# Kernel optimization log

Measured on AMD Instinct MI355X. Metric: run time of the kernel, lower is better.

The kernel has to match this reference:

```python
import jax, jax.numpy as jnp
import numpy as np

V, CTX, D, L, H = 50257, 2048, 768, 12, 12
HD = D // H
EPS = 1e-5


def _ln(x, w, b):
    mu = jnp.mean(x, axis=-1, keepdims=True)
    var = jnp.mean(jnp.square(x - mu), axis=-1, keepdims=True)
    return (x - mu) * jax.lax.rsqrt(var + EPS) * w + b


def setup_inputs() -> dict:
    key = jax.random.key(0)
    ks = jax.random.split(key, 8)
    s = 0.02  # init std, matches _init_weights
    return {
        "idx": jax.random.randint(ks[0], (2, 2048), 0, V),
        "wte": jax.random.normal(ks[1], (V, D), jnp.float32) * s,
        "wpe": jax.random.normal(ks[2], (CTX, D), jnp.float32) * s,
        "ln1_w": jnp.ones((L, D), jnp.float32),
        "ln1_b": jnp.zeros((L, D), jnp.float32),
        "qkv_w": jax.random.normal(ks[3], (L, 3 * D, D), jnp.float32) * s,
        "out_w": jax.random.normal(ks[4], (L, D, D), jnp.float32) * s,
        "ln2_w": jnp.ones((L, D), jnp.float32),
        "ln2_b": jnp.zeros((L, D), jnp.float32),
        "fc1_w": jax.random.normal(ks[5], (L, 4 * D, D), jnp.float32) * s,
        "fc2_w": jax.random.normal(ks[6], (L, D, 4 * D), jnp.float32) * s,
        "lnf_w": jnp.ones((D,), jnp.float32),
        "lnf_b": jnp.zeros((D,), jnp.float32),
    }


def reference(idx, wte, wpe, ln1_w, ln1_b, qkv_w, out_w, ln2_w, ln2_b,
              fc1_w, fc2_w, lnf_w, lnf_b):
    B, S = idx.shape
    x = wte[idx] + wpe[:S][None]  # [B,S,D]
    causal = jnp.tril(jnp.ones((S, S), bool))  # [S,S]
    scale = 1.0 / np.sqrt(HD)

    def block(x, p):
        l1w, l1b, qkvw, ow, l2w, l2b, f1w, f2w = p
        h = _ln(x, l1w, l1b)
        qkv = h @ qkvw.T  # [B,S,3D]
        q, k, v = jnp.split(qkv, 3, axis=-1)
        q = q.reshape(B, S, H, HD)
        k = k.reshape(B, S, H, HD)
        v = v.reshape(B, S, H, HD)
        scores = jnp.einsum("bqhd,bkhd->bhqk", q, k) * scale
        scores = jnp.where(causal, scores, -jnp.inf)
        attn = jax.nn.softmax(scores, axis=-1)
        ctx = jnp.einsum("bhqk,bkhd->bqhd", attn, v).reshape(B, S, D)
        x = x + ctx @ ow.T
        h2 = _ln(x, l2w, l2b)
        mlp = jax.nn.gelu(h2 @ f1w.T, approximate=False) @ f2w.T
        return x + mlp, None

    x, _ = jax.lax.scan(block, x, (ln1_w, ln1_b, qkv_w, out_w, ln2_w, ln2_b, fc1_w, fc2_w))
    x = _ln(x, lnf_w, lnf_b)
    logits = x @ wte.T  # tied lm_head
    return logits
```

## Files before the change

### kernel.cpp

```cpp
#include <hip/hip_runtime.h>
#include <hip/hip_bf16.h>
#include <math.h>

typedef __attribute__((ext_vector_type(4))) float f32x4;
typedef __attribute__((ext_vector_type(8))) short bf16x8;
typedef __attribute__((ext_vector_type(4))) float float4v;
typedef unsigned short u16;
typedef unsigned int u32;

#define DIM 768
#define SEQ 2048
#define NTOK 4096
#define NH 12
#define NL 12
#define VOCAB 50257

__device__ __forceinline__ u16 f2bf(float f) {
  union { float f; u32 u; } c; c.f = f;
  u32 u = c.u;
  u32 r = u + 0x7fffu + ((u >> 16) & 1u);
  return (u16)(r >> 16);
}

__device__ __forceinline__ float fexp2(float x) {
#if __has_builtin(__builtin_amdgcn_exp2f)
  return __builtin_amdgcn_exp2f(x);
#else
  return exp2f(x);
#endif
}

__device__ __forceinline__ f32x4 mfma_bf16(bf16x8 a, bf16x8 b, f32x4 c) {
  return __builtin_amdgcn_mfma_f32_16x16x32_bf16(a, b, c, 0, 0, 0);
}

__device__ __forceinline__ void gload_lds16(const u16* g, u16* l) {
  __builtin_amdgcn_global_load_lds((const __attribute__((address_space(1))) u32*)g,
                                   (__attribute__((address_space(3))) u32*)l, 16, 0, 0);
}

__global__ void embed_k(const int* __restrict__ idx, const float* __restrict__ wte,
                        const float* __restrict__ wpe, float* __restrict__ x) {
  int t = blockIdx.x * 256 + threadIdx.x;
  int n = t / 192, c = t % 192;
  int tok = idx[n];
  float4v a = ((const float4v*)wte)[(size_t)tok * 192 + c];
  float4v p = ((const float4v*)wpe)[(size_t)(n & (SEQ - 1)) * 192 + c];
  ((float4v*)x)[t] = a + p;
}

__global__ __launch_bounds__(256) void ln_k(const float* __restrict__ x,
                                            const float* __restrict__ w,
                                            const float* __restrict__ b,
                                            u16* __restrict__ out) {
  int lane = threadIdx.x & 63;
  int row = blockIdx.x * 4 + (threadIdx.x >> 6);
  const float4v* xr = (const float4v*)(x + (size_t)row * DIM);
  float4v v[3];
#pragma unroll
  for (int i = 0; i < 3; ++i) v[i] = xr[i * 64 + lane];
  float s = 0.f;
#pragma unroll
  for (int i = 0; i < 3; ++i)
#pragma unroll
    for (int j = 0; j < 4; ++j) s += v[i][j];
#pragma unroll
  for (int o = 1; o < 64; o <<= 1) s += __shfl_xor(s, o);
  float mu = s * (1.f / 768.f);
  float vs = 0.f;
#pragma unroll
  for (int i = 0; i < 3; ++i)
#pragma unroll
    for (int j = 0; j < 4; ++j) { float d = v[i][j] - mu; vs += d * d; }
#pragma unroll
  for (int o = 1; o < 64; o <<= 1) vs += __shfl_xor(vs, o);
  float rs = rsqrtf(vs * (1.f / 768.f) + 1e-5f);
  u16* orow = out + (size_t)row * DIM;
#pragma unroll
  for (int i = 0; i < 3; ++i) {
    float4v wv = ((const float4v*)w)[i * 64 + lane];
    float4v bv = ((const float4v*)b)[i * 64 + lane];
    float y0 = (v[i][0] - mu) * rs * wv[0] + bv[0];
    float y1 = (v[i][1] - mu) * rs * wv[1] + bv[1];
    float y2 = (v[i][2] - mu) * rs * wv[2] + bv[2];
    float y3 = (v[i][3] - mu) * rs * wv[3] + bv[3];
    uint2 pk;
    pk.x = (u32)f2bf(y0) | ((u32)f2bf(y1) << 16);
    pk.y = (u32)f2bf(y2) | ((u32)f2bf(y3) << 16);
    ((uint2*)orow)[i * 64 + lane] = pk;
  }
}

__global__ void cvt_k(const float* __restrict__ src, u16* __restrict__ dst, int n4) {
  int stride = gridDim.x * blockDim.x;
  for (int i = blockIdx.x * blockDim.x + threadIdx.x; i < n4; i += stride) {
    float4v v = ((const float4v*)src)[i];
    uint2 pk;
    pk.x = (u32)f2bf(v[0]) | ((u32)f2bf(v[1]) << 16);
    pk.y = (u32)f2bf(v[2]) | ((u32)f2bf(v[3]) << 16);
    ((uint2*)dst)[i] = pk;
  }
}

template <int EPI>
__global__ __launch_bounds__(256) void gemm128p(const u16* __restrict__ A,
                                                const u16* __restrict__ W, int Mdim,
                                                int Kdim, u16* __restrict__ outb,
                                                float* __restrict__ resid) {
  __shared__ u16 lA[2][128 * 64];
  __shared__ u16 lW[2][128 * 64];
  const int m0 = blockIdx.y * 128;
  const int n0 = blockIdx.x * 128;
  const int tid = threadIdx.x;
  const int lane = tid & 63, wv = tid >> 6;
  const int wr = wv >> 1, wc = wv & 1;
  const int lr = lane & 15, hi = lane >> 4;

  f32x4 acc[4][4];
#pragma unroll
  for (int i = 0; i < 4; ++i)
#pragma unroll
    for (int j = 0; j < 4; ++j) acc[i][j] = (f32x4){0.f, 0.f, 0.f, 0.f};

  const int s_row = tid >> 3;
  const int s_col = (tid & 7) * 8;
  const int g_col = s_col ^ ((s_row & 7) << 3);
  int wrow[4];
#pragma unroll
  for (int it = 0; it < 4; ++it) {
    int r = m0 + s_row + it * 32;
    wrow[it] = (r < Mdim) ? r : (Mdim - 1);
  }

  const int nt = Kdim >> 6;

  auto stage = [&](int kt, int buf) {
    const int k0 = kt * 64;
#pragma unroll
    for (int it = 0; it < 4; ++it) {
      gload_lds16(A + (size_t)(n0 + s_row + it * 32) * Kdim + k0 + g_col,
                  &lA[buf][(s_row + it * 32) * 64 + s_col]);
      gload_lds16(W + (size_t)wrow[it] * Kdim + k0 + g_col,
                  &lW[buf][(s_row + it * 32) * 64 + s_col]);
    }
  };

  const int swz = (lr & 7) << 3;

  stage(0, 0);
  stage(1, 1);
  asm volatile("s_waitcnt vmcnt(8)" ::: "memory");
  __builtin_amdgcn_s_barrier();

  for (int t = 0; t < nt; ++t) {
    const int cur = t & 1;
    const u16* la = lA[cur];
    const u16* lw = lW[cur];
#pragma unroll
    for (int kk = 0; kk < 2; ++kk) {
      const int csw = (kk * 32 + hi * 8) ^ swz;
      bf16x8 af[4], wf[4];
#pragma unroll
      for (int i = 0; i < 4; ++i)
        af[i] = *(const bf16x8*)(&la[(wr * 64 + i * 16 + lr) * 64 + csw]);
#pragma unroll
      for (int j = 0; j < 4; ++j)
        wf[j] = *(const bf16x8*)(&lw[(wc * 64 + j * 16 + lr) * 64 + csw]);
      __builtin_amdgcn_s_setprio(1);
#pragma unroll
      for (int i = 0; i < 4; ++i)
#pragma unroll
        for (int j = 0; j < 4; ++j) acc[i][j] = mfma_bf16(af[i], wf[j], acc[i][j]);
      __builtin_amdgcn_s_setprio(0);
    }
    __builtin_amdgcn_s_barrier();
    if (t + 2 < nt) {
      stage(t + 2, cur);
      asm volatile("s_waitcnt vmcnt(8)" ::: "memory");
    } else if (t + 1 < nt) {
      asm volatile("s_waitcnt vmcnt(0)" ::: "memory");
    }
    __builtin_amdgcn_s_barrier();
  }

#pragma unroll
  for (int i = 0; i < 4; ++i) {
#pragma unroll
    for (int j = 0; j < 4; ++j) {
      int nb = n0 + wr * 64 + i * 16 + hi * 4;
      int m = m0 + wc * 64 + j * 16 + lr;
#pragma unroll
      for (int r = 0; r < 4; ++r) {
        float val = acc[i][j][r];
        size_t o = (size_t)(nb + r) * Mdim + m;
        if (EPI == 0) {
          if (m < Mdim) outb[o] = f2bf(val);
        } else if (EPI == 1) {
          float g = 0.5f * val * (1.f + erff(val * 0.70710678118f));
          outb[o] = f2bf(g);
        } else if (EPI == 2) {
          resid[o] += val;
        } else {
          if (m < Mdim) resid[o] = val;
        }
      }
    }
  }
}

template <int EPI>
__global__ __launch_bounds__(512) void gemm256(const u16* __restrict__ A,
                                               const u16* __restrict__ W, int Mdim,
                                               int Kdim, u16* __restrict__ outb,
                                               float* __restrict__ resid) {
  __shared__ u16 lA[2][256 * 64];
  __shared__ u16 lB[2][256 * 64];
  const int n0 = blockIdx.x * 256;
  const int m0 = blockIdx.y * 256;
  const int tid = threadIdx.x;
  const int lane = tid & 63, wid = tid >> 6;
  const int wr = wid >> 2, wc = wid & 3;
  const int lr = lane & 15, hi = lane >> 4;

  const int s_row = tid >> 3;
  const int s_col = (tid & 7) * 8;
  const int g_col = s_col ^ ((s_row & 7) << 3);
  int wrow[4];
#pragma unroll
  for (int it = 0; it < 4; ++it) {
    int r = m0 + s_row + it * 64;
    wrow[it] = (r < Mdim) ? r : (Mdim - 1);
  }

  f32x4 acc[8][4];
#pragma unroll
  for (int i = 0; i < 8; ++i)
#pragma unroll
    for (int j = 0; j < 4; ++j) acc[i][j] = (f32x4){0.f, 0.f, 0.f, 0.f};

  const int nt = Kdim >> 6;

  auto stage = [&](int kt, int buf) {
    const int k0 = kt * 64;
#pragma unroll
    for (int it = 0; it < 4; ++it)
      gload_lds16(A + (size_t)(n0 + s_row + it * 64) * Kdim + k0 + g_col,
                  &lA[buf][(s_row + it * 64) * 64 + s_col]);
#pragma unroll
    for (int it = 0; it < 4; ++it)
      gload_lds16(W + (size_t)wrow[it] * Kdim + k0 + g_col,
                  &lB[buf][(s_row + it * 64) * 64 + s_col]);
  };

  const int swz = (lr & 7) << 3;

  stage(0, 0);
  stage(1, 1);
  asm volatile("s_waitcnt vmcnt(8)" ::: "memory");
  __builtin_amdgcn_s_barrier();

  for (int t = 0; t < nt; ++t) {
    const int cur = t & 1;
    const u16* la = lA[cur];
    const u16* lb = lB[cur];
#pragma unroll
    for (int kk = 0; kk < 2; ++kk) {
      const int csw = (kk * 32 + hi * 8) ^ swz;
      bf16x8 af[8], wf[4];
#pragma unroll
      for (int i = 0; i < 8; ++i)
        af[i] = *(const bf16x8*)(&la[(wr * 128 + i * 16 + lr) * 64 + csw]);
#pragma unroll
      for (int j = 0; j < 4; ++j)
        wf[j] = *(const bf16x8*)(&lb[(wc * 64 + j * 16 + lr) * 64 + csw]);
      __builtin_amdgcn_s_setprio(1);
#pragma unroll
      for (int i = 0; i < 8; ++i)
#pragma unroll
        for (int j = 0; j < 4; ++j) acc[i][j] = mfma_bf16(af[i], wf[j], acc[i][j]);
      __builtin_amdgcn_s_setprio(0);
    }
    __builtin_amdgcn_s_barrier();
    if (t + 2 < nt) {
      stage(t + 2, cur);
      asm volatile("s_waitcnt vmcnt(8)" ::: "memory");
    } else if (t + 1 < nt) {
      asm volatile("s_waitcnt vmcnt(0)" ::: "memory");
    }
    __builtin_amdgcn_s_barrier();
  }

#pragma unroll
  for (int i = 0; i < 8; ++i) {
#pragma unroll
    for (int j = 0; j < 4; ++j) {
      int nb = n0 + wr * 128 + i * 16 + hi * 4;
      int m = m0 + wc * 64 + j * 16 + lr;
#pragma unroll
      for (int r = 0; r < 4; ++r) {
        float val = acc[i][j][r];
        size_t o = (size_t)(nb + r) * Mdim + m;
        if (EPI == 0) {
          if (m < Mdim) outb[o] = f2bf(val);
        } else if (EPI == 1) {
          float g = 0.5f * val * (1.f + erff(val * 0.70710678118f));
          outb[o] = f2bf(g);
        } else {
          if (m < Mdim) resid[o] = val;
        }
      }
    }
  }
}

__global__ __launch_bounds__(256) void vtrans_k(const u16* __restrict__ qkv,
                                                u16* __restrict__ vT) {
  __shared__ u16 t[64][65];
  int bh = blockIdx.y;
  int b = bh / NH, h = bh % NH;
  int s0 = blockIdx.x * 64;
  int tid = threadIdx.x;
  int col = tid & 63, row0 = tid >> 6;
#pragma unroll
  for (int it = 0; it < 16; ++it) {
    int srow = row0 + it * 4;
    t[srow][col] = qkv[(size_t)(b * SEQ + s0 + srow) * 2304 + 1536 + h * 64 + col];
  }
  __syncthreads();
#pragma unroll
  for (int it = 0; it < 16; ++it) {
    int drow = row0 + it * 4;
    vT[((size_t)bh * 64 + drow) * SEQ + s0 + col] = t[col][drow];
  }
}

__global__ __launch_bounds__(512) void flash_k(const u16* __restrict__ qkv,
                                               const u16* __restrict__ vT,
                                               u16* __restrict__ ctx) {
  const int tid = threadIdx.x;
  const int lane = tid & 63, wq = tid >> 6;
  const int lr = lane & 15, hi = lane >> 4;
  const int pi = blockIdx.x;
  const int bh = blockIdx.y;
  const int b = bh / NH, h = bh % NH;
  const size_t rowb = (size_t)b * SEQ;
  const float SCL = 0.125f * 1.44269504f;

  __shared__ u16 lK[64 * 80];
  __shared__ u16 lV[64 * 80];
  __shared__ u16 Pb[8][16 * 40];
  u16* P = Pb[wq];

  const int s_row = tid >> 3;
  const int s_col = (tid & 7) * 8;
  const u16* kSrc = qkv + rowb * 2304 + 768 + h * 64;
  const u16* vSrc = vT + ((size_t)bh * 64 + s_row) * SEQ;

#pragma unroll
  for (int pass = 0; pass < 2; ++pass) {
    const int qb = (pass == 0 ? (15 - pi) : pi) * 128;
    const int qa = qb + wq * 16;

    const u16* Qp = qkv + (rowb + qa + lr) * 2304 + h * 64 + hi * 8;
    bf16x8 qf0 = *(const bf16x8*)(Qp);
    bf16x8 qf1 = *(const bf16x8*)(Qp + 32);

    f32x4 o[4];
    float mreg[4], lreg[4];
#pragma unroll
    for (int ct = 0; ct < 4; ++ct) o[ct] = (f32x4){0.f, 0.f, 0.f, 0.f};
#pragma unroll
    for (int r = 0; r < 4; ++r) { mreg[r] = -1e30f; lreg[r] = 0.f; }

    const int kTop = qb + 127;
    bf16x8 kreg = *(const bf16x8*)(kSrc + (size_t)s_row * 2304 + s_col);
    bf16x8 vreg = *(const bf16x8*)(vSrc + s_col);

    for (int k0 = 0; k0 <= kTop; k0 += 64) {
      __syncthreads();
      *(bf16x8*)(&lK[s_row * 80 + s_col]) = kreg;
      *(bf16x8*)(&lV[s_row * 80 + s_col]) = vreg;
      __syncthreads();
      if (k0 + 64 <= kTop) {
        kreg = *(const bf16x8*)(kSrc + (size_t)(k0 + 64 + s_row) * 2304 + s_col);
        vreg = *(const bf16x8*)(vSrc + k0 + 64 + s_col);
      }
      if (k0 <= qa + 15) {
#pragma unroll
        for (int ks = 0; ks < 2; ++ks) {
          const int kg = k0 + ks * 32;
          f32x4 s0 = (f32x4){0.f, 0.f, 0.f, 0.f}, s1 = (f32x4){0.f, 0.f, 0.f, 0.f};
          {
            bf16x8 ka = *(const bf16x8*)(&lK[(ks * 32 + lr) * 80 + hi * 8]);
            bf16x8 kc = *(const bf16x8*)(&lK[(ks * 32 + lr) * 80 + hi * 8 + 32]);
            s0 = mfma_bf16(qf0, ka, s0);
            s0 = mfma_bf16(qf1, kc, s0);
            bf16x8 kd = *(const bf16x8*)(&lK[(ks * 32 + 16 + lr) * 80 + hi * 8]);
            bf16x8 ke = *(const bf16x8*)(&lK[(ks * 32 + 16 + lr) * 80 + hi * 8 + 32]);
            s1 = mfma_bf16(qf0, kd, s1);
            s1 = mfma_bf16(qf1, ke, s1);
          }
          float cor[4];
#pragma unroll
          for (int r = 0; r < 4; ++r) {
            int qrow = qa + hi * 4 + r;
            float v0 = s0[r] * SCL;
            if (kg + lr > qrow) v0 = -1e30f;
            float v1 = s1[r] * SCL;
            if (kg + 16 + lr > qrow) v1 = -1e30f;
            s0[r] = v0; s1[r] = v1;
            float m = fmaxf(v0, v1);
            m = fmaxf(m, __shfl_xor(m, 1));
            m = fmaxf(m, __shfl_xor(m, 2));
            m = fmaxf(m, __shfl_xor(m, 4));
            m = fmaxf(m, __shfl_xor(m, 8));
            float mnew = fmaxf(mreg[r], m);
            cor[r] = fexp2(mreg[r] - mnew);
            mreg[r] = mnew;
          }
#pragma unroll
          for (int r = 0; r < 4; ++r) {
            float p0 = fexp2(s0[r] - mreg[r]);
            float p1 = fexp2(s1[r] - mreg[r]);
            lreg[r] = lreg[r] * cor[r] + p0 + p1;
            P[(hi * 4 + r) * 40 + lr] = f2bf(p0);
            P[(hi * 4 + r) * 40 + 16 + lr] = f2bf(p1);
#pragma unroll
            for (int ct = 0; ct < 4; ++ct) o[ct][r] *= cor[r];
          }
          bf16x8 pa = *(const bf16x8*)(&P[lr * 40 + hi * 8]);
#pragma unroll
          for (int ct = 0; ct < 4; ++ct) {
            bf16x8 vf = *(const bf16x8*)(&lV[(ct * 16 + lr) * 80 + ks * 32 + hi * 8]);
            o[ct] = mfma_bf16(pa, vf, o[ct]);
          }
        }
      }
    }

    float lfin[4];
#pragma unroll
    for (int r = 0; r < 4; ++r) {
      float l = lreg[r];
      l += __shfl_xor(l, 1);
      l += __shfl_xor(l, 2);
      l += __shfl_xor(l, 4);
      l += __shfl_xor(l, 8);
      lfin[r] = 1.f / l;
    }
#pragma unroll
    for (int ct = 0; ct < 4; ++ct)
#pragma unroll
      for (int r = 0; r < 4; ++r) {
        float ov = o[ct][r] * lfin[r];
        size_t n = rowb + qa + hi * 4 + r;
        ctx[n * DIM + h * 64 + ct * 16 + lr] = f2bf(ov);
      }
  }
}

extern "C" void kernel_launch(void* const* d_in, const int* in_sizes, int n_in,
                              void* d_out, int out_size, void* d_ws, size_t ws_size,
                              hipStream_t stream) {
  (void)in_sizes; (void)n_in; (void)out_size; (void)ws_size;
  const int* idx = (const int*)d_in[0];
  const float* wte = (const float*)d_in[1];
  const float* wpe = (const float*)d_in[2];
  const float* ln1w = (const float*)d_in[3];
  const float* ln1b = (const float*)d_in[4];
  const float* qkvw = (const float*)d_in[5];
  const float* outw = (const float*)d_in[6];
  const float* ln2w = (const float*)d_in[7];
  const float* ln2b = (const float*)d_in[8];
  const float* fc1w = (const float*)d_in[9];
  const float* fc2w = (const float*)d_in[10];
  const float* lnfw = (const float*)d_in[11];
  const float* lnfb = (const float*)d_in[12];
  float* out = (float*)d_out;

  char* ws = (char*)d_ws;
  size_t off = 0;
  auto carve = [&](size_t bytes) {
    char* p = ws + off;
    off += (bytes + 255) & ~(size_t)255;
    return p;
  };
  u16* hb = (u16*)carve((size_t)NTOK * DIM * 2);
  u16* wteb = (u16*)carve((size_t)VOCAB * DIM * 2);

  char* os = (char*)d_out;
  size_t ooff = 0;
  auto ocarve = [&](size_t bytes) {
    char* p = os + ooff;
    ooff += (bytes + 255) & ~(size_t)255;
    return p;
  };
  float* xb = (float*)ocarve((size_t)NTOK * DIM * 4);
  u16* qkvb = (u16*)ocarve((size_t)NTOK * 3 * DIM * 2);
  u16* ctxb = (u16*)ocarve((size_t)NTOK * DIM * 2);
  u16* mhb = (u16*)ocarve((size_t)NTOK * 4 * DIM * 2);
  u16* vTb = (u16*)ocarve((size_t)2 * NH * 64 * SEQ * 2);
  u16* qkvwb = (u16*)ocarve((size_t)NL * 1769472 * 2);
  u16* outwb = (u16*)ocarve((size_t)NL * 589824 * 2);
  u16* fc1wb = (u16*)ocarve((size_t)NL * 2359296 * 2);
  u16* fc2wb = (u16*)ocarve((size_t)NL * 2359296 * 2);

  cvt_k<<<2048, 256, 0, stream>>>(qkvw, qkvwb, NL * 442368);
  cvt_k<<<2048, 256, 0, stream>>>(outw, outwb, NL * 147456);
  cvt_k<<<2048, 256, 0, stream>>>(fc1w, fc1wb, NL * 589824);
  cvt_k<<<2048, 256, 0, stream>>>(fc2w, fc2wb, NL * 589824);
  cvt_k<<<2048, 256, 0, stream>>>(wte, wteb, 9649344);

  embed_k<<<3072, 256, 0, stream>>>(idx, wte, wpe, xb);

  for (int l = 0; l < NL; ++l) {
    ln_k<<<1024, 256, 0, stream>>>(xb, ln1w + l * DIM, ln1b + l * DIM, hb);
    gemm256<0><<<dim3(16, 9), 512, 0, stream>>>(hb, qkvwb + (size_t)l * 1769472,
                                                2304, 768, qkvb, nullptr);
    vtrans_k<<<dim3(32, 24), 256, 0, stream>>>(qkvb, vTb);
    flash_k<<<dim3(8, 24), 512, 0, stream>>>(qkvb, vTb, ctxb);
    gemm128p<2><<<dim3(32, 6), 256, 0, stream>>>(ctxb, outwb + (size_t)l * 589824,
                                                 768, 768, nullptr, xb);
    ln_k<<<1024, 256, 0, stream>>>(xb, ln2w + l * DIM, ln2b + l * DIM, hb);
    gemm256<1><<<dim3(16, 12), 512, 0, stream>>>(hb, fc1wb + (size_t)l * 2359296,
                                                 3072, 768, mhb, nullptr);
    gemm128p<2><<<dim3(32, 6), 256, 0, stream>>>(mhb, fc2wb + (size_t)l * 2359296,
                                                 768, 3072, nullptr, xb);
  }

  ln_k<<<1024, 256, 0, stream>>>(xb, lnfw, lnfb, hb);
  gemm256<3><<<dim3(16, 197), 512, 0, stream>>>(hb, wteb, VOCAB, 768, nullptr, out);
}
```

Before: 3.979 ms.

## Restructure flash attention to 32-row waves and use 128-tile GEMMs for QKV/FC1

The flash kernel drops the two-pass pairing of query tiles. Each block now handles one 128-row query tile with 4 waves of 32 rows each, so every K/V fragment loaded from LDS is reused across two 16-row MFMA groups. The grid is flattened to 384 blocks ordered heaviest-first for causal load balance. The QKV and FC1 projections also switch from the 256-tile GEMM to the 128-tile gemm128p variant, giving more blocks to fill the CUs at the cost of less reuse per tile.

```diff
diff --git a/kernel.cpp b/kernel.cpp
--- a/kernel.cpp
+++ b/kernel.cpp
@@ -334,129 +334,175 @@
   }
 }
 
-__global__ __launch_bounds__(512) void flash_k(const u16* __restrict__ qkv,
+__global__ __launch_bounds__(256) void flash_k(const u16* __restrict__ qkv,
                                                const u16* __restrict__ vT,
                                                u16* __restrict__ ctx) {
   const int tid = threadIdx.x;
   const int lane = tid & 63, wq = tid >> 6;
   const int lr = lane & 15, hi = lane >> 4;
-  const int pi = blockIdx.x;
-  const int bh = blockIdx.y;
+  const int bx = blockIdx.x;
+  const int qt = 15 - (bx / 24);
+  const int bh = bx % 24;
   const int b = bh / NH, h = bh % NH;
+  const int qb = qt * 128;
+  const int qa = qb + wq * 32;
   const size_t rowb = (size_t)b * SEQ;
   const float SCL = 0.125f * 1.44269504f;
 
   __shared__ u16 lK[64 * 80];
   __shared__ u16 lV[64 * 80];
-  __shared__ u16 Pb[8][16 * 40];
-  u16* P = Pb[wq];
+  __shared__ u16 Pb[4][2][16 * 40];
+  u16* P0 = &Pb[wq][0][0];
+  u16* P1 = &Pb[wq][1][0];
 
   const int s_row = tid >> 3;
   const int s_col = (tid & 7) * 8;
   const u16* kSrc = qkv + rowb * 2304 + 768 + h * 64;
-  const u16* vSrc = vT + ((size_t)bh * 64 + s_row) * SEQ;
-
-#pragma unroll
-  for (int pass = 0; pass < 2; ++pass) {
-    const int qb = (pass == 0 ? (15 - pi) : pi) * 128;
-    const int qa = qb + wq * 16;
-
-    const u16* Qp = qkv + (rowb + qa + lr) * 2304 + h * 64 + hi * 8;
-    bf16x8 qf0 = *(const bf16x8*)(Qp);
-    bf16x8 qf1 = *(const bf16x8*)(Qp + 32);
-
-    f32x4 o[4];
-    float mreg[4], lreg[4];
-#pragma unroll
-    for (int ct = 0; ct < 4; ++ct) o[ct] = (f32x4){0.f, 0.f, 0.f, 0.f};
-#pragma unroll
-    for (int r = 0; r < 4; ++r) { mreg[r] = -1e30f; lreg[r] = 0.f; }
-
-    const int kTop = qb + 127;
-    bf16x8 kreg = *(const bf16x8*)(kSrc + (size_t)s_row * 2304 + s_col);
-    bf16x8 vreg = *(const bf16x8*)(vSrc + s_col);
-
-    for (int k0 = 0; k0 <= kTop; k0 += 64) {
-      __syncthreads();
-      *(bf16x8*)(&lK[s_row * 80 + s_col]) = kreg;
-      *(bf16x8*)(&lV[s_row * 80 + s_col]) = vreg;
-      __syncthreads();
-      if (k0 + 64 <= kTop) {
-        kreg = *(const bf16x8*)(kSrc + (size_t)(k0 + 64 + s_row) * 2304 + s_col);
-        vreg = *(const bf16x8*)(vSrc + k0 + 64 + s_col);
-      }
-      if (k0 <= qa + 15) {
-#pragma unroll
-        for (int ks = 0; ks < 2; ++ks) {
-          const int kg = k0 + ks * 32;
-          f32x4 s0 = (f32x4){0.f, 0.f, 0.f, 0.f}, s1 = (f32x4){0.f, 0.f, 0.f, 0.f};
-          {
-            bf16x8 ka = *(const bf16x8*)(&lK[(ks * 32 + lr) * 80 + hi * 8]);
-            bf16x8 kc = *(const bf16x8*)(&lK[(ks * 32 + lr) * 80 + hi * 8 + 32]);
-            s0 = mfma_bf16(qf0, ka, s0);
-            s0 = mfma_bf16(qf1, kc, s0);
-            bf16x8 kd = *(const bf16x8*)(&lK[(ks * 32 + 16 + lr) * 80 + hi * 8]);
-            bf16x8 ke = *(const bf16x8*)(&lK[(ks * 32 + 16 + lr) * 80 + hi * 8 + 32]);
-            s1 = mfma_bf16(qf0, kd, s1);
-            s1 = mfma_bf16(qf1, ke, s1);
-          }
+  const u16* vSrcA = vT + ((size_t)bh * 64 + s_row) * SEQ;
+  const u16* vSrcB = vT + ((size_t)bh * 64 + s_row + 32) * SEQ;
+
+  const u16* Qp = qkv + (rowb + qa + lr) * 2304 + h * 64 + hi * 8;
+  bf16x8 qf00 = *(const bf16x8*)(Qp);
+  bf16x8 qf01 = *(const bf16x8*)(Qp + 32);
+  bf16x8 qf10 = *(const bf16x8*)(Qp + 16 * 2304);
+  bf16x8 qf11 = *(const bf16x8*)(Qp + 16 * 2304 + 32);
+
+  f32x4 o0[4], o1[4];
+  float m0[4], l0[4], m1[4], l1[4];
+#pragma unroll
+  for (int ct = 0; ct < 4; ++ct) {
+    o0[ct] = (f32x4){0.f, 0.f, 0.f, 0.f};
+    o1[ct] = (f32x4){0.f, 0.f, 0.f, 0.f};
+  }
+#pragma unroll
+  for (int r = 0; r < 4; ++r) { m0[r] = -1e30f; l0[r] = 0.f; m1[r] = -1e30f; l1[r] = 0.f; }
+
+  const int kTop = qb + 127;
+  bf16x8 kr0 = *(const bf16x8*)(kSrc + (size_t)s_row * 2304 + s_col);
+  bf16x8 kr1 = *(const bf16x8*)(kSrc + (size_t)(s_row + 32) * 2304 + s_col);
+  bf16x8 vr0 = *(const bf16x8*)(vSrcA + s_col);
+  bf16x8 vr1 = *(const bf16x8*)(vSrcB + s_col);
+
+  for (int k0 = 0; k0 <= kTop; k0 += 64) {
+    __syncthreads();
+    *(bf16x8*)(&lK[s_row * 80 + s_col]) = kr0;
+    *(bf16x8*)(&lK[(s_row + 32) * 80 + s_col]) = kr1;
+    *(bf16x8*)(&lV[s_row * 80 + s_col]) = vr0;
+    *(bf16x8*)(&lV[(s_row + 32) * 80 + s_col]) = vr1;
+    __syncthreads();
+    if (k0 + 64 <= kTop) {
+      kr0 = *(const bf16x8*)(kSrc + (size_t)(k0 + 64 + s_row) * 2304 + s_col);
+      kr1 = *(const bf16x8*)(kSrc + (size_t)(k0 + 96 + s_row) * 2304 + s_col);
+      vr0 = *(const bf16x8*)(vSrcA + k0 + 64 + s_col);
+      vr1 = *(const bf16x8*)(vSrcB + k0 + 64 + s_col);
+    }
+    if (k0 <= qa + 31) {
+#pragma unroll
+      for (int ks = 0; ks < 2; ++ks) {
+        const int kg = k0 + ks * 32;
+        if (kg > qa + 31) continue;
+        bf16x8 ka = *(const bf16x8*)(&lK[(ks * 32 + lr) * 80 + hi * 8]);
+        bf16x8 kc = *(const bf16x8*)(&lK[(ks * 32 + lr) * 80 + hi * 8 + 32]);
+        bf16x8 kd = *(const bf16x8*)(&lK[(ks * 32 + 16 + lr) * 80 + hi * 8]);
+        bf16x8 ke = *(const bf16x8*)(&lK[(ks * 32 + 16 + lr) * 80 + hi * 8 + 32]);
+        f32x4 sA0 = (f32x4){0.f, 0.f, 0.f, 0.f}, sA1 = (f32x4){0.f, 0.f, 0.f, 0.f};
+        f32x4 sB0 = (f32x4){0.f, 0.f, 0.f, 0.f}, sB1 = (f32x4){0.f, 0.f, 0.f, 0.f};
+        sA0 = mfma_bf16(qf00, ka, sA0); sA0 = mfma_bf16(qf01, kc, sA0);
+        sA1 = mfma_bf16(qf00, kd, sA1); sA1 = mfma_bf16(qf01, ke, sA1);
+        sB0 = mfma_bf16(qf10, ka, sB0); sB0 = mfma_bf16(qf11, kc, sB0);
+        sB1 = mfma_bf16(qf10, kd, sB1); sB1 = mfma_bf16(qf11, ke, sB1);
+        {
           float cor[4];
 #pragma unroll
           for (int r = 0; r < 4; ++r) {
             int qrow = qa + hi * 4 + r;
-            float v0 = s0[r] * SCL;
+            float v0 = sA0[r] * SCL;
             if (kg + lr > qrow) v0 = -1e30f;
-            float v1 = s1[r] * SCL;
+            float v1 = sA1[r] * SCL;
             if (kg + 16 + lr > qrow) v1 = -1e30f;
-            s0[r] = v0; s1[r] = v1;
+            sA0[r] = v0; sA1[r] = v1;
             float m = fmaxf(v0, v1);
             m = fmaxf(m, __shfl_xor(m, 1));
             m = fmaxf(m, __shfl_xor(m, 2));
             m = fmaxf(m, __shfl_xor(m, 4));
             m = fmaxf(m, __shfl_xor(m, 8));
-            float mnew = fmaxf(mreg[r], m);
-            cor[r] = fexp2(mreg[r] - mnew);
-            mreg[r] = mnew;
+            float mnew = fmaxf(m0[r], m);
+            cor[r] = fexp2(m0[r] - mnew);
+            m0[r] = mnew;
           }
 #pragma unroll
           for (int r = 0; r < 4; ++r) {
-            float p0 = fexp2(s0[r] - mreg[r]);
-            float p1 = fexp2(s1[r] - mreg[r]);
-            lreg[r] = lreg[r] * cor[r] + p0 + p1;
-            P[(hi * 4 + r) * 40 + lr] = f2bf(p0);
-            P[(hi * 4 + r) * 40 + 16 + lr] = f2bf(p1);
-#pragma unroll
-            for (int ct = 0; ct < 4; ++ct) o[ct][r] *= cor[r];
-          }
-          bf16x8 pa = *(const bf16x8*)(&P[lr * 40 + hi * 8]);
-#pragma unroll
-          for (int ct = 0; ct < 4; ++ct) {
-            bf16x8 vf = *(const bf16x8*)(&lV[(ct * 16 + lr) * 80 + ks * 32 + hi * 8]);
-            o[ct] = mfma_bf16(pa, vf, o[ct]);
+            float p0 = fexp2(sA0[r] - m0[r]);
+            float p1 = fexp2(sA1[r] - m0[r]);
+            l0[r] = l0[r] * cor[r] + p0 + p1;
+            P0[(hi * 4 + r) * 40 + lr] = f2bf(p0);
+            P0[(hi * 4 + r) * 40 + 16 + lr] = f2bf(p1);
+#pragma unroll
+            for (int ct = 0; ct < 4; ++ct) o0[ct][r] *= cor[r];
           }
         }
+        {
+          float cor[4];
+#pragma unroll
+          for (int r = 0; r < 4; ++r) {
+            int qrow = qa + 16 + hi * 4 + r;
+            float v0 = sB0[r] * SCL;
+            if (kg + lr > qrow) v0 = -1e30f;
+            float v1 = sB1[r] * SCL;
+            if (kg + 16 + lr > qrow) v1 = -1e30f;
+            sB0[r] = v0; sB1[r] = v1;
+            float m = fmaxf(v0, v1);
+            m = fmaxf(m, __shfl_xor(m, 1));
+            m = fmaxf(m, __shfl_xor(m, 2));
+            m = fmaxf(m, __shfl_xor(m, 4));
+            m = fmaxf(m, __shfl_xor(m, 8));
+            float mnew = fmaxf(m1[r], m);
+            cor[r] = fexp2(m1[r] - mnew);
+            m1[r] = mnew;
+          }
+#pragma unroll
+          for (int r = 0; r < 4; ++r) {
+            float p0 = fexp2(sB0[r] - m1[r]);
+            float p1 = fexp2(sB1[r] - m1[r]);
+            l1[r] = l1[r] * cor[r] + p0 + p1;
+            P1[(hi * 4 + r) * 40 + lr] = f2bf(p0);
+            P1[(hi * 4 + r) * 40 + 16 + lr] = f2bf(p1);
+#pragma unroll
+            for (int ct = 0; ct < 4; ++ct) o1[ct][r] *= cor[r];
+          }
+        }
+        bf16x8 pa0 = *(const bf16x8*)(&P0[lr * 40 + hi * 8]);
+        bf16x8 pa1 = *(const bf16x8*)(&P1[lr * 40 + hi * 8]);
+#pragma unroll
+        for (int ct = 0; ct < 4; ++ct) {
+          bf16x8 vf = *(const bf16x8*)(&lV[(ct * 16 + lr) * 80 + ks * 32 + hi * 8]);
+          o0[ct] = mfma_bf16(pa0, vf, o0[ct]);
+          o1[ct] = mfma_bf16(pa1, vf, o1[ct]);
+        }
       }
     }
-
-    float lfin[4];
+  }
+
+  float lf0[4], lf1[4];
+#pragma unroll
+  for (int r = 0; r < 4; ++r) {
+    float la = l0[r];
+    la += __shfl_xor(la, 1); la += __shfl_xor(la, 2);
+    la += __shfl_xor(la, 4); la += __shfl_xor(la, 8);
+    lf0[r] = 1.f / la;
+    float lb = l1[r];
+    lb += __shfl_xor(lb, 1); lb += __shfl_xor(lb, 2);
+    lb += __shfl_xor(lb, 4); lb += __shfl_xor(lb, 8);
+    lf1[r] = 1.f / lb;
+  }
+#pragma unroll
+  for (int ct = 0; ct < 4; ++ct)
 #pragma unroll
     for (int r = 0; r < 4; ++r) {
-      float l = lreg[r];
-      l += __shfl_xor(l, 1);
-      l += __shfl_xor(l, 2);
-      l += __shfl_xor(l, 4);
-      l += __shfl_xor(l, 8);
-      lfin[r] = 1.f / l;
-    }
-#pragma unroll
-    for (int ct = 0; ct < 4; ++ct)
-#pragma unroll
-      for (int r = 0; r < 4; ++r) {
-        float ov = o[ct][r] * lfin[r];
-        size_t n = rowb + qa + hi * 4 + r;
-        ctx[n * DIM + h * 64 + ct * 16 + lr] = f2bf(ov);
-      }
-  }
+      size_t n = rowb + qa + hi * 4 + r;
+      ctx[n * DIM + h * 64 + ct * 16 + lr] = f2bf(o0[ct][r] * lf0[r]);
+      ctx[(n + 16) * DIM + h * 64 + ct * 16 + lr] = f2bf(o1[ct][r] * lf1[r]);
+    }
 }
 
 extern "C" void kernel_launch(void* const* d_in, const int* in_sizes, int n_in,
@@ -515,15 +561,15 @@
 
   for (int l = 0; l < NL; ++l) {
     ln_k<<<1024, 256, 0, stream>>>(xb, ln1w + l * DIM, ln1b + l * DIM, hb);
-    gemm256<0><<<dim3(16, 9), 512, 0, stream>>>(hb, qkvwb + (size_t)l * 1769472,
-                                                2304, 768, qkvb, nullptr);
+    gemm128p<0><<<dim3(32, 18), 256, 0, stream>>>(hb, qkvwb + (size_t)l * 1769472,
+                                                  2304, 768, qkvb, nullptr);
     vtrans_k<<<dim3(32, 24), 256, 0, stream>>>(qkvb, vTb);
-    flash_k<<<dim3(8, 24), 512, 0, stream>>>(qkvb, vTb, ctxb);
+    flash_k<<<384, 256, 0, stream>>>(qkvb, vTb, ctxb);
     gemm128p<2><<<dim3(32, 6), 256, 0, stream>>>(ctxb, outwb + (size_t)l * 589824,
                                                  768, 768, nullptr, xb);
     ln_k<<<1024, 256, 0, stream>>>(xb, ln2w + l * DIM, ln2b + l * DIM, hb);
-    gemm256<1><<<dim3(16, 12), 512, 0, stream>>>(hb, fc1wb + (size_t)l * 2359296,
-                                                 3072, 768, mhb, nullptr);
+    gemm128p<1><<<dim3(32, 24), 256, 0, stream>>>(hb, fc1wb + (size_t)l * 2359296,
+                                                  3072, 768, mhb, nullptr);
     gemm128p<2><<<dim3(32, 6), 256, 0, stream>>>(mhb, fc2wb + (size_t)l * 2359296,
                                                  768, 3072, nullptr, xb);
   }
```

Result: slower. 4.535 ms (+14.0%).
